# Performance work log

Hardware: AMD Instinct MI355X
Metric: run time of the kernel (lower is better)

The kernel has to match this reference:

```python
import jax, jax.numpy as jnp
import numpy as np

DIM = 768
HEADS = 12
B, NV, NQ, NA = 32, 100, 32, 32


def setup_inputs() -> dict:
    key = jax.random.key(0)
    ks = jax.random.split(key, 18)
    inp = {
        "v": jax.random.normal(ks[0], (B, NV, DIM), jnp.float32),
        "q": jax.random.normal(ks[1], (B, NQ, DIM), jnp.float32),
        "a": jax.random.normal(ks[2], (B, NA, DIM), jnp.float32),
        "v_mask": jax.random.randint(ks[3], (B, NV), 0, 2, jnp.int32),
        "q_mask": jax.random.randint(ks[4], (B, NQ), 0, 2, jnp.int32),
        "a_mask": jax.random.randint(ks[5], (B, NA), 0, 2, jnp.int32),
    }
    names = ["Wv", "bv", "Wq", "bq", "Wa", "ba", "Wvo", "bvo", "Wqo", "bqo", "Wao", "bao"]
    for i, n in enumerate(names):
        shape = (DIM, DIM) if n.startswith("W") else (DIM,)
        inp[n] = jax.random.normal(ks[6 + i], shape, jnp.float32) * 0.02
    return inp


def _heads(x):
    # (B, S, DIM) -> (B, H, S, W)
    b, s, _ = x.shape
    return x.reshape(b, s, HEADS, DIM // HEADS).transpose(0, 2, 1, 3)


def reference(v, q, a, v_mask, q_mask, a_mask,
              Wv, bv, Wq, bq, Wa, ba, Wvo, bvo, Wqo, bqo, Wao, bao):
    # projections; note: *_out projections are applied to the already-projected tensors
    vp = v @ Wv + bv
    qp = q @ Wq + bq
    ap = a @ Wa + ba
    vo = vp @ Wvo + bvo
    qo = qp @ Wqo + bqo
    ao = ap @ Wao + bao

    vh, qh, ah = _heads(vp), _heads(qp), _heads(ap)          # (B,H,S,W)
    voh, qoh, aoh = _heads(vo), _heads(qo), _heads(ao)

    dh = DIM // HEADS
    scale = 1.0 / float(np.sqrt(dh))
    # trilinear scores: (B,H,V,Q,A)
    att = jnp.einsum('bhvw,bhqw,bhaw->bhvqa', vh, qh, ah) * scale
    att = att - 10000.0 * v_mask[:, None, :, None, None].astype(att.dtype)
    att = att - 10000.0 * q_mask[:, None, None, :, None].astype(att.dtype)
    att = att - 10000.0 * a_mask[:, None, None, None, :].astype(att.dtype)

    # softmax over the flattened joint (V*Q*A) axis, per (batch, head)
    att = jax.nn.softmax(att.reshape(B, HEADS, NV * NQ * NA), axis=-1)
    att = att.reshape(B, HEADS, NV, NQ, NA)  # dropout: eval mode (identity)

    v_out = jnp.einsum('bhvqa,bhvw->bvhw', att, voh).reshape(B, NV, DIM)
    q_out = jnp.einsum('bhvqa,bhqw->bqhw', att, qoh).reshape(B, NQ, DIM)
    a_out = jnp.einsum('bhvqa,bhaw->bahw', att, aoh).reshape(B, NA, DIM)
    return (v_out, q_out, a_out)
```

## Files before the change

kernel.cpp:

```cpp
#include <hip/hip_runtime.h>
#include <hip/hip_bf16.h>

#define DIM 768
#define NH  12
#define HW  64
#define BB  32
#define NV  100
#define NQ  32
#define NA  32

#define VP_ELEMS (BB * NV * DIM)
#define QP_ELEMS (BB * NQ * DIM)
#define AP_ELEMS (BB * NA * DIM)
#define S1 (VP_ELEMS)
#define S2 (S1 + QP_ELEMS)
#define STOT (S2 + AP_ELEMS)
#define WELEMS (DIM * DIM)
#define NBH (BB * NH)
#define PREP_BLOCKS (864 + BB)
#define NROWS (BB * (NV + NQ + NA))

typedef __attribute__((ext_vector_type(8))) short     bf16x8;
typedef __attribute__((ext_vector_type(8))) unsigned short u16x8;
typedef __attribute__((ext_vector_type(4))) float     f32x4;

__device__ __forceinline__ float bf16r(float x) {
    return __bfloat162float(__float2bfloat16(x));
}
__device__ __forceinline__ unsigned short f2bu(float x) {
    __hip_bfloat16 h = __float2bfloat16(x);
    return *reinterpret_cast<unsigned short*>(&h);
}
__device__ __forceinline__ float bu2f(unsigned short u) {
    union { unsigned int i; float f; } c;
    c.i = ((unsigned int)u) << 16;
    return c.f;
}

__global__ __launch_bounds__(256) void prep(
    const float* __restrict__ W0, const float* __restrict__ W1,
    const float* __restrict__ W2, const float* __restrict__ W3,
    const float* __restrict__ W4, const float* __restrict__ W5,
    unsigned short* __restrict__ WtAll,
    const int* __restrict__ vmask, const int* __restrict__ qmask, const int* __restrict__ amask,
    int* __restrict__ vidx_g, int* __restrict__ qidx_g, int* __restrict__ aidx_g,
    int* __restrict__ vbase_g, int* __restrict__ qbase_g, int* __restrict__ abase_g,
    int* __restrict__ rv_list, int* __restrict__ rq_list, int* __restrict__ ra_list,
    int* __restrict__ tot_g,
    float* __restrict__ out)
{
    const int tid = threadIdx.x;

#pragma unroll
    for (int it = 0; it < 5; ++it) {
        const int e4 = blockIdx.x * 256 + tid + it * (PREP_BLOCKS * 256);
        const int i = e4 * 4;
        if (i < STOT) *(float4*)&out[i] = float4{0.f, 0.f, 0.f, 0.f};
    }

    if (blockIdx.x < 864) {
        __shared__ float tile[64][65];
        const int widx = blockIdx.x / 144;
        const int t    = blockIdx.x % 144;
        const int tr = t / 12, tc = t % 12;
        const float* W = (widx == 0) ? W0 : (widx == 1) ? W1 : (widx == 2) ? W2
                       : (widx == 3) ? W3 : (widx == 4) ? W4 : W5;
        unsigned short* Wt = WtAll + (size_t)widx * WELEMS;
        const int c = tid & 63, r4 = tid >> 6;
#pragma unroll
        for (int it = 0; it < 16; ++it) {
            int r = it * 4 + r4;
            tile[r][c] = W[(size_t)(tr * 64 + r) * DIM + tc * 64 + c];
        }
        __syncthreads();
#pragma unroll
        for (int it = 0; it < 16; ++it) {
            int r = it * 4 + r4;
            Wt[(size_t)(tc * 64 + r) * DIM + tr * 64 + c] = f2bu(tile[c][r]);
        }
        return;
    }

    const int b = blockIdx.x - 864;
    __shared__ int cv[BB], cq[BB], ca[BB];
    __shared__ int bs[3];

    if (tid < BB) {
        int s = 0;
        for (int i = 0; i < NV; ++i) s += (vmask[tid * NV + i] == 0);
        cv[tid] = s;
    } else if (tid >= 64 && tid < 64 + BB) {
        const int bb = tid - 64;
        int s = 0;
        for (int i = 0; i < NQ; ++i) s += (qmask[bb * NQ + i] == 0);
        cq[bb] = s;
    } else if (tid >= 128 && tid < 128 + BB) {
        const int bb = tid - 128;
        int s = 0;
        for (int i = 0; i < NA; ++i) s += (amask[bb * NA + i] == 0);
        ca[bb] = s;
    }
    __syncthreads();

    if (tid == 0) {
        int sv = 0, sq = 0, sa = 0;
        for (int j = 0; j < b; ++j) { sv += cv[j]; sq += cq[j]; sa += ca[j]; }
        bs[0] = sv; bs[1] = sq; bs[2] = sa;
        vbase_g[b] = sv; qbase_g[b] = sq; abase_g[b] = sa;
    }
    if (b == 0 && tid == 1) {
        int sv = 0, sq = 0, sa = 0;
        for (int j = 0; j < BB; ++j) { sv += cv[j]; sq += cq[j]; sa += ca[j]; }
        vbase_g[BB] = sv; qbase_g[BB] = sq; abase_g[BB] = sa;
        tot_g[0] = sv; tot_g[1] = sq; tot_g[2] = sa;
    }
    __syncthreads();
    const int basev = bs[0], baseq = bs[1], basea = bs[2];

    const int lane = tid & 63, w = tid >> 6;
    __shared__ int c0sh;
    const bool mv = (tid < NV) && (vmask[b * NV + tid] == 0);
    const unsigned long long bal = __ballot(mv);
    const int pre = __popcll(bal & ((1ull << lane) - 1ull));
    if (w == 0 && lane == 0) c0sh = __popcll(bal);
    __syncthreads();
    const int vbloc = (w == 0) ? 0 : c0sh;
    if (mv) {
        vidx_g[b * NV + vbloc + pre] = tid;
        rv_list[basev + vbloc + pre] = b * NV + tid;
    }
    const bool mq = (w == 0) && (lane < NQ) && (qmask[b * NQ + lane] == 0);
    const unsigned long long balq = __ballot(mq);
    if (mq) {
        const int preq = __popcll(balq & ((1ull << lane) - 1ull));
        qidx_g[b * NQ + preq] = lane;
        rq_list[baseq + preq] = b * NQ + lane;
    }
    const bool ma = (w == 1) && (lane < NA) && (amask[b * NA + lane] == 0);
    const unsigned long long bala = __ballot(ma);
    if (ma) {
        const int prea = __popcll(bala & ((1ull << lane) - 1ull));
        aidx_g[b * NA + prea] = lane;
        ra_list[basea + prea] = b * NA + lane;
    }
}

__global__ __launch_bounds__(256) void gemm_proj(
    const float* __restrict__ X0, const float* __restrict__ X1, const float* __restrict__ X2,
    const unsigned short* __restrict__ W0, const unsigned short* __restrict__ W1,
    const unsigned short* __restrict__ W2,
    const float* __restrict__ c0, const float* __restrict__ c1, const float* __restrict__ c2,
    unsigned short* __restrict__ Y0, unsigned short* __restrict__ Y1,
    unsigned short* __restrict__ Y2,
    const int* __restrict__ rv_list, const int* __restrict__ rq_list, const int* __restrict__ ra_list,
    const int* __restrict__ tot_g)
{
    __shared__ unsigned short As[64 * 32];
    __shared__ unsigned short Bs[128 * 32];

    const int t = blockIdx.x;
    int set, loc;
    if (t < 300)      { set = 0; loc = t; }
    else if (t < 396) { set = 1; loc = t - 300; }
    else              { set = 2; loc = t - 396; }
    const int tm = loc / 6, tn = loc % 6;
    const int cnt = tot_g[set];
    const int bm = tm * 64, bn = tn * 128;
    if (bm >= cnt) return;

    const float* Xf          = (set == 0) ? X0 : (set == 1) ? X1 : X2;
    const unsigned short* Wt = (set == 0) ? W0 : (set == 1) ? W1 : W2;
    const float* bias        = (set == 0) ? c0 : (set == 1) ? c1 : c2;
    unsigned short* Y        = (set == 0) ? Y0 : (set == 1) ? Y1 : Y2;
    const int* rlist         = (set == 0) ? rv_list : (set == 1) ? rq_list : ra_list;

    const int tid = threadIdx.x, lane = tid & 63, wave = tid >> 6;
    const int col = lane & 15, rg = lane >> 4;

    const int arow = tid >> 2, akc = (tid & 3) << 3;
    const int brow = tid >> 1, bkc = (tid & 1) << 4;
    const int grow = bm + arow;
    const int asrc = (grow < cnt) ? rlist[grow] : 0;

    f32x4 acc[4][2] = {};

    for (int k0 = 0; k0 < DIM; k0 += 32) {
        u16x8 u = {};
        if (grow < cnt) {
            const float4 f0 = *(const float4*)&Xf[(size_t)asrc * DIM + k0 + akc];
            const float4 f1 = *(const float4*)&Xf[(size_t)asrc * DIM + k0 + akc + 4];
            u[0] = f2bu(f0.x); u[1] = f2bu(f0.y); u[2] = f2bu(f0.z); u[3] = f2bu(f0.w);
            u[4] = f2bu(f1.x); u[5] = f2bu(f1.y); u[6] = f2bu(f1.z); u[7] = f2bu(f1.w);
        }
        *(u16x8*)&As[arow * 32 + akc] = u;
        *(u16x8*)&Bs[brow * 32 + bkc] =
            *(const u16x8*)&Wt[(size_t)(bn + brow) * DIM + k0 + bkc];
        *(u16x8*)&Bs[brow * 32 + bkc + 8] =
            *(const u16x8*)&Wt[(size_t)(bn + brow) * DIM + k0 + bkc + 8];
        __syncthreads();

        bf16x8 af[4], bfr[2];
#pragma unroll
        for (int mi = 0; mi < 4; ++mi)
            af[mi] = *(const bf16x8*)&As[(mi * 16 + col) * 32 + rg * 8];
#pragma unroll
        for (int ni = 0; ni < 2; ++ni)
            bfr[ni] = *(const bf16x8*)&Bs[(wave * 32 + ni * 16 + col) * 32 + rg * 8];
#pragma unroll
        for (int mi = 0; mi < 4; ++mi)
#pragma unroll
            for (int ni = 0; ni < 2; ++ni)
                acc[mi][ni] = __builtin_amdgcn_mfma_f32_16x16x32_bf16(
                    af[mi], bfr[ni], acc[mi][ni], 0, 0, 0);
        __syncthreads();
    }

#pragma unroll
    for (int mi = 0; mi < 4; ++mi) {
#pragma unroll
        for (int r = 0; r < 4; ++r) {
            const int m = bm + mi * 16 + rg * 4 + r;
            if (m >= cnt) continue;
#pragma unroll
            for (int ni = 0; ni < 2; ++ni) {
                const int n = bn + wave * 32 + ni * 16 + col;
                Y[(size_t)m * DIM + n] = f2bu(acc[mi][ni][r] + bias[n]);
            }
        }
    }
}

__global__ __launch_bounds__(256, 2) void outmm_marginal(
    const unsigned short* __restrict__ vpb, const unsigned short* __restrict__ qpb,
    const unsigned short* __restrict__ apb,
    const unsigned short* __restrict__ W3, const unsigned short* __restrict__ W4,
    const unsigned short* __restrict__ W5,
    const float* __restrict__ bvo, const float* __restrict__ bqo, const float* __restrict__ bao,
    unsigned short* __restrict__ ov, unsigned short* __restrict__ oq, unsigned short* __restrict__ oa,
    const int* __restrict__ vbase_g, const int* __restrict__ qbase_g, const int* __restrict__ abase_g,
    const int* __restrict__ vidx_g, const int* __restrict__ qidx_g, const int* __restrict__ aidx_g,
    float* __restrict__ pv, float* __restrict__ pq, float* __restrict__ pa,
    const int* __restrict__ tot_g)
{
    const int tid = threadIdx.x, lane = tid & 63, wave = tid >> 6;
    const int col = lane & 15, rg = lane >> 4;

    if (blockIdx.x < 492) {
        __shared__ unsigned short As[64 * 32];
        __shared__ unsigned short Bs[128 * 32];
        const int t = blockIdx.x;
        int set, loc;
        if (t < 300)      { set = 0; loc = t; }
        else if (t < 396) { set = 1; loc = t - 300; }
        else              { set = 2; loc = t - 396; }
        const int tm = loc / 6, tn = loc % 6;
        const int cnt = tot_g[set];
        const int bm = tm * 64, bn = tn * 128;
        if (bm >= cnt) return;

        const unsigned short* Xb = (set == 0) ? vpb : (set == 1) ? qpb : apb;
        const unsigned short* Wt = (set == 0) ? W3 : (set == 1) ? W4 : W5;
        const float* bias        = (set == 0) ? bvo : (set == 1) ? bqo : bao;
        unsigned short* Y        = (set == 0) ? ov : (set == 1) ? oq : oa;

        const int arow = tid >> 2, akc = (tid & 3) << 3;
        const int brow = tid >> 1, bkc = (tid & 1) << 4;
        const int grow = bm + arow;

        f32x4 acc[4][2] = {};
        for (int k0 = 0; k0 < DIM; k0 += 32) {
            *(u16x8*)&As[arow * 32 + akc] =
                *(const u16x8*)&Xb[(size_t)grow * DIM + k0 + akc];
            *(u16x8*)&Bs[brow * 32 + bkc] =
                *(const u16x8*)&Wt[(size_t)(bn + brow) * DIM + k0 + bkc];
            *(u16x8*)&Bs[brow * 32 + bkc + 8] =
                *(const u16x8*)&Wt[(size_t)(bn + brow) * DIM + k0 + bkc + 8];
            __syncthreads();

            bf16x8 af[4], bfr[2];
#pragma unroll
            for (int mi = 0; mi < 4; ++mi)
                af[mi] = *(const bf16x8*)&As[(mi * 16 + col) * 32 + rg * 8];
#pragma unroll
            for (int ni = 0; ni < 2; ++ni)
                bfr[ni] = *(const bf16x8*)&Bs[(wave * 32 + ni * 16 + col) * 32 + rg * 8];
#pragma unroll
            for (int mi = 0; mi < 4; ++mi)
#pragma unroll
                for (int ni = 0; ni < 2; ++ni)
                    acc[mi][ni] = __builtin_amdgcn_mfma_f32_16x16x32_bf16(
                        af[mi], bfr[ni], acc[mi][ni], 0, 0, 0);
            __syncthreads();
        }

#pragma unroll
        for (int mi = 0; mi < 4; ++mi) {
#pragma unroll
            for (int r = 0; r < 4; ++r) {
                const int m = bm + mi * 16 + rg * 4 + r;
                if (m >= cnt) continue;
#pragma unroll
                for (int ni = 0; ni < 2; ++ni) {
                    const int n = bn + wave * 32 + ni * 16 + col;
                    Y[(size_t)m * DIM + n] = f2bu(acc[mi][ni][r] + bias[n]);
                }
            }
        }
        return;
    }

    const int bh = blockIdx.x - 492;
    const int b = bh / NH, h = bh % NH;

    __shared__ unsigned short vhs[112 * 72];
    __shared__ unsigned short qhs[NQ * 72];
    __shared__ unsigned short ahs[NA * 72];
    __shared__ float aoff[NA];
    __shared__ float pv_sh[112], pa_sh[NA], pq_sh[NQ];
    __shared__ float zsh;

    const int vb0 = vbase_g[b], vcnt = vbase_g[b + 1] - vb0;
    const int qb0 = qbase_g[b], qcnt = qbase_g[b + 1] - qb0;
    const int ab0 = abase_g[b], acnt = abase_g[b + 1] - ab0;

    if (tid < 112) pv_sh[tid] = 0.f;
    if (tid < NA)  { aoff[tid] = (tid < acnt) ? 0.f : -200.f; pa_sh[tid] = 0.f; }

    for (int i = tid >> 3; i < vcnt; i += 32) {
        const int c = tid & 7;
        *(u16x8*)&vhs[i * 72 + c * 8] =
            *(const u16x8*)&vpb[(size_t)(vb0 + i) * DIM + h * 64 + c * 8];
    }
    {
        const int pr = vcnt + (tid >> 3);
        if ((tid >> 3) < 16 && pr < 112) {
            const int c = tid & 7;
            u16x8 z = {};
            *(u16x8*)&vhs[pr * 72 + c * 8] = z;
        }
    }
    for (int i = tid >> 3; i < qcnt; i += 32) {
        const int c = tid & 7;
        *(u16x8*)&qhs[i * 72 + c * 8] =
            *(const u16x8*)&qpb[(size_t)(qb0 + i) * DIM + h * 64 + c * 8];
    }
    for (int i = tid >> 3; i < acnt; i += 32) {
        const int c = tid & 7;
        *(u16x8*)&ahs[i * 72 + c * 8] =
            *(const u16x8*)&apb[(size_t)(ab0 + i) * DIM + h * 64 + c * 8];
    }
    {
        const int pr = acnt + (tid >> 3);
        if ((tid >> 3) < 16 && pr < NA) {
            const int c = tid & 7;
            u16x8 z = {};
            *(u16x8*)&ahs[pr * 72 + c * 8] = z;
        }
    }
    __syncthreads();

    const int nvt = (vcnt + 15) >> 4;
    const int nat = (acnt + 15) >> 4;

    float pvacc[7][4] = {};
    float za0 = 0.f, za1 = 0.f;
    const float sc2 = 0.125f * 1.44269504088896f;

    for (int qs = wave; qs < qcnt; qs += 4) {
        float zq = 0.f;
#pragma unroll
        for (int ah = 0; ah < 2; ++ah) {
            if (ah < nat) {
                const int ai = (ah << 4) + col;
                const u16x8 qv0 = *(const u16x8*)&qhs[qs * 72 + rg * 8];
                const u16x8 qv1 = *(const u16x8*)&qhs[qs * 72 + 32 + rg * 8];
                const u16x8 av0 = *(const u16x8*)&ahs[ai * 72 + rg * 8];
                const u16x8 av1 = *(const u16x8*)&ahs[ai * 72 + 32 + rg * 8];
                bf16x8 bf0, bf1;
#pragma unroll
                for (int j = 0; j < 8; ++j) {
                    bf0[j] = (short)f2bu(bu2f(qv0[j]) * bu2f(av0[j]));
                    bf1[j] = (short)f2bu(bu2f(qv1[j]) * bu2f(av1[j]));
                }
                const float poff = aoff[ai];
                float ts = 0.f;
#pragma unroll
                for (int vt = 0; vt < 7; ++vt) {
                    if (vt < nvt) {
                        const bf16x8 a0 = *(const bf16x8*)&vhs[(vt * 16 + col) * 72 + rg * 8];
                        const bf16x8 a1 = *(const bf16x8*)&vhs[(vt * 16 + col) * 72 + 32 + rg * 8];
                        f32x4 acc = {};
                        acc = __builtin_amdgcn_mfma_f32_16x16x32_bf16(a0, bf0, acc, 0, 0, 0);
                        acc = __builtin_amdgcn_mfma_f32_16x16x32_bf16(a1, bf1, acc, 0, 0, 0);
                        if ((vt + 1) * 16 <= vcnt) {
#pragma unroll
                            for (int r = 0; r < 4; ++r) {
                                const float e = exp2f(fmaf(acc[r], sc2, poff));
                                pvacc[vt][r] += e;
                                ts += e;
                            }
                        } else {
#pragma unroll
                            for (int r = 0; r < 4; ++r) {
                                const float off = (vt * 16 + rg * 4 + r < vcnt) ? poff : -200.f;
                                const float e = exp2f(fmaf(acc[r], sc2, off));
                                pvacc[vt][r] += e;
                                ts += e;
                            }
                        }
                    }
                }
                if (ah) za1 += ts; else za0 += ts;
                zq += ts;
            }
        }
        zq += __shfl_xor(zq, 1);  zq += __shfl_xor(zq, 2);  zq += __shfl_xor(zq, 4);
        zq += __shfl_xor(zq, 8);  zq += __shfl_xor(zq, 16); zq += __shfl_xor(zq, 32);
        if (lane == 0) pq_sh[qs] = zq;
    }

#pragma unroll
    for (int vt = 0; vt < 7; ++vt) {
        if (vt < nvt) {
#pragma unroll
            for (int r = 0; r < 4; ++r) {
                float x = pvacc[vt][r];
                x += __shfl_xor(x, 1); x += __shfl_xor(x, 2);
                x += __shfl_xor(x, 4); x += __shfl_xor(x, 8);
                if (col == 0) atomicAdd(&pv_sh[vt * 16 + rg * 4 + r], x);
            }
        }
    }
    {
        float x = za0;
        x += __shfl_xor(x, 16); x += __shfl_xor(x, 32);
        if (rg == 0) atomicAdd(&pa_sh[col], x);
        float y = za1;
        y += __shfl_xor(y, 16); y += __shfl_xor(y, 32);
        if (rg == 0) atomicAdd(&pa_sh[16 + col], y);
    }
    __syncthreads();

    if (tid < 64) {
        float x = (lane < qcnt) ? pq_sh[lane] : 0.f;
        x += __shfl_xor(x, 1); x += __shfl_xor(x, 2); x += __shfl_xor(x, 4);
        x += __shfl_xor(x, 8); x += __shfl_xor(x, 16); x += __shfl_xor(x, 32);
        if (lane == 0) zsh = x;
    }
    if (tid < NV) pv[bh * NV + tid] = 0.f;
    if (tid < NQ) pq[bh * NQ + tid] = 0.f;
    if (tid < NA) pa[bh * NA + tid] = 0.f;
    __syncthreads();
    const float invZ = 1.0f / zsh;
    if (tid < vcnt) pv[bh * NV + vidx_g[b * NV + tid]] = pv_sh[tid] * invZ;
    if (tid < qcnt) pq[bh * NQ + qidx_g[b * NQ + tid]] = pq_sh[tid] * invZ;
    if (tid < acnt) pa[bh * NA + aidx_g[b * NA + tid]] = pa_sh[tid] * invZ;
}

__global__ __launch_bounds__(192) void scale_out(
    const unsigned short* __restrict__ ov, const unsigned short* __restrict__ oq,
    const unsigned short* __restrict__ oa,
    const float* __restrict__ pv, const float* __restrict__ pq, const float* __restrict__ pa,
    const int* __restrict__ rv_list, const int* __restrict__ rq_list, const int* __restrict__ ra_list,
    const int* __restrict__ tot_g, float* __restrict__ out)
{
    const int t0 = tot_g[0], t1 = tot_g[1], t2 = tot_g[2];
    int m = blockIdx.x;
    const unsigned short* ob; const float* mg; const int* rl; int S; float* os;
    if (m < t0)           { ob = ov; mg = pv; rl = rv_list; S = NV; os = out; }
    else if (m < t0 + t1) { m -= t0; ob = oq; mg = pq; rl = rq_list; S = NQ; os = out + S1; }
    else if (m < t0 + t1 + t2) { m -= t0 + t1; ob = oa; mg = pa; rl = ra_list; S = NA; os = out + S2; }
    else return;

    const int src = rl[m];
    const int bb = src / S, ss = src - bb * S;
    const int n = threadIdx.x * 4;
    const int h = n >> 6;
    const float mgv = mg[(bb * NH + h) * S + ss];
    const ushort4 u = *(const ushort4*)&ob[(size_t)m * DIM + n];
    float4 o;
    o.x = bf16r(bu2f(u.x) * mgv);
    o.y = bf16r(bu2f(u.y) * mgv);
    o.z = bf16r(bu2f(u.z) * mgv);
    o.w = bf16r(bu2f(u.w) * mgv);
    *(float4*)&os[(size_t)src * DIM + n] = o;
}

extern "C" void kernel_launch(void* const* d_in, const int* in_sizes, int n_in,
                              void* d_out, int out_size, void* d_ws, size_t ws_size,
                              hipStream_t stream)
{
    const float* v     = (const float*)d_in[0];
    const float* q     = (const float*)d_in[1];
    const float* a     = (const float*)d_in[2];
    const int*   vmask = (const int*)d_in[3];
    const int*   qmask = (const int*)d_in[4];
    const int*   amask = (const int*)d_in[5];
    const float* Wv  = (const float*)d_in[6];
    const float* bv  = (const float*)d_in[7];
    const float* Wq  = (const float*)d_in[8];
    const float* bq  = (const float*)d_in[9];
    const float* Wa  = (const float*)d_in[10];
    const float* ba  = (const float*)d_in[11];
    const float* Wvo = (const float*)d_in[12];
    const float* bvo = (const float*)d_in[13];
    const float* Wqo = (const float*)d_in[14];
    const float* bqo = (const float*)d_in[15];
    const float* Wao = (const float*)d_in[16];
    const float* bao = (const float*)d_in[17];
    float* out = (float*)d_out;

    unsigned short* wsu = (unsigned short*)d_ws;
    unsigned short* WtAll = wsu;
    unsigned short* vpb   = WtAll + 6 * WELEMS;
    unsigned short* qpb   = vpb + VP_ELEMS;
    unsigned short* apb   = qpb + QP_ELEMS;
    unsigned short* ov    = apb + AP_ELEMS;
    unsigned short* oq    = ov + VP_ELEMS;
    unsigned short* oa    = oq + QP_ELEMS;
    float* fbase   = (float*)(oa + AP_ELEMS);
    float* pv      = fbase;
    float* pq      = pv + NBH * NV;
    float* pa      = pq + NBH * NQ;
    int* vidx_g    = (int*)(pa + NBH * NA);
    int* qidx_g    = vidx_g + BB * NV;
    int* aidx_g    = qidx_g + BB * NQ;
    int* vbase_g   = aidx_g + BB * NA;
    int* qbase_g   = vbase_g + BB + 1;
    int* abase_g   = qbase_g + BB + 1;
    int* rv_list   = abase_g + BB + 1;
    int* rq_list   = rv_list + BB * NV;
    int* ra_list   = rq_list + BB * NQ;
    int* tot_g     = ra_list + BB * NA;

    prep<<<dim3(PREP_BLOCKS), dim3(256), 0, stream>>>(
        Wv, Wq, Wa, Wvo, Wqo, Wao, WtAll,
        vmask, qmask, amask,
        vidx_g, qidx_g, aidx_g, vbase_g, qbase_g, abase_g,
        rv_list, rq_list, ra_list, tot_g, out);

    gemm_proj<<<dim3(492), dim3(256), 0, stream>>>(
        v, q, a,
        WtAll + 0 * WELEMS, WtAll + 1 * WELEMS, WtAll + 2 * WELEMS,
        bv, bq, ba,
        vpb, qpb, apb,
        rv_list, rq_list, ra_list, tot_g);

    outmm_marginal<<<dim3(492 + NBH), dim3(256), 0, stream>>>(
        vpb, qpb, apb,
        WtAll + 3 * WELEMS, WtAll + 4 * WELEMS, WtAll + 5 * WELEMS,
        bvo, bqo, bao,
        ov, oq, oa,
        vbase_g, qbase_g, abase_g,
        vidx_g, qidx_g, aidx_g,
        pv, pq, pa, tot_g);

    scale_out<<<dim3(NROWS), dim3(192), 0, stream>>>(
        ov, oq, oa, pv, pq, pa,
        rv_list, rq_list, ra_list, tot_g, out);
}
```

Measured before the change: 67.86 us.

## Defer output-weight conversion and output zeroing into the projection GEMM launch

The prep kernel now converts only the three input projection weights. The conversion of the three output weights and the zeroing of the output buffer move into extra blocks of the gemm_proj launch, so they run alongside the projection GEMM. This shortens the serial prep stage on the critical path. In exchange, the GEMM blocks share the GPU with the conversion blocks and also take on part of the zeroing stores.

Measured after the change: 65.87 us. 2.9% less time.

```diff
diff --git a/kernel.cpp b/kernel.cpp
--- a/kernel.cpp
+++ b/kernel.cpp
@@ -17,8 +17,8 @@
 #define STOT (S2 + AP_ELEMS)
 #define WELEMS (DIM * DIM)
 #define NBH (BB * NH)
-#define PREP_BLOCKS (864 + BB)
 #define NROWS (BB * (NV + NQ + NA))
+#define P2_BLOCKS (492 + 432)
 
 typedef __attribute__((ext_vector_type(8))) short     bf16x8;
 typedef __attribute__((ext_vector_type(8))) unsigned short u16x8;
@@ -37,51 +37,45 @@
     return c.f;
 }
 
+__device__ __forceinline__ void conv_tile(
+    const float* __restrict__ W, unsigned short* __restrict__ Wt, int t, int tid)
+{
+    __shared__ float tile[64][65];
+    const int tr = t / 12, tc = t % 12;
+    const int c = tid & 63, r4 = tid >> 6;
+#pragma unroll
+    for (int it = 0; it < 16; ++it) {
+        int r = it * 4 + r4;
+        tile[r][c] = W[(size_t)(tr * 64 + r) * DIM + tc * 64 + c];
+    }
+    __syncthreads();
+#pragma unroll
+    for (int it = 0; it < 16; ++it) {
+        int r = it * 4 + r4;
+        Wt[(size_t)(tc * 64 + r) * DIM + tr * 64 + c] = f2bu(tile[c][r]);
+    }
+}
+
 __global__ __launch_bounds__(256) void prep(
     const float* __restrict__ W0, const float* __restrict__ W1,
-    const float* __restrict__ W2, const float* __restrict__ W3,
-    const float* __restrict__ W4, const float* __restrict__ W5,
+    const float* __restrict__ W2,
     unsigned short* __restrict__ WtAll,
     const int* __restrict__ vmask, const int* __restrict__ qmask, const int* __restrict__ amask,
     int* __restrict__ vidx_g, int* __restrict__ qidx_g, int* __restrict__ aidx_g,
     int* __restrict__ vbase_g, int* __restrict__ qbase_g, int* __restrict__ abase_g,
     int* __restrict__ rv_list, int* __restrict__ rq_list, int* __restrict__ ra_list,
-    int* __restrict__ tot_g,
-    float* __restrict__ out)
+    int* __restrict__ tot_g)
 {
     const int tid = threadIdx.x;
 
-#pragma unroll
-    for (int it = 0; it < 5; ++it) {
-        const int e4 = blockIdx.x * 256 + tid + it * (PREP_BLOCKS * 256);
-        const int i = e4 * 4;
-        if (i < STOT) *(float4*)&out[i] = float4{0.f, 0.f, 0.f, 0.f};
-    }
-
-    if (blockIdx.x < 864) {
-        __shared__ float tile[64][65];
+    if (blockIdx.x < 432) {
         const int widx = blockIdx.x / 144;
-        const int t    = blockIdx.x % 144;
-        const int tr = t / 12, tc = t % 12;
-        const float* W = (widx == 0) ? W0 : (widx == 1) ? W1 : (widx == 2) ? W2
-                       : (widx == 3) ? W3 : (widx == 4) ? W4 : W5;
-        unsigned short* Wt = WtAll + (size_t)widx * WELEMS;
-        const int c = tid & 63, r4 = tid >> 6;
-#pragma unroll
-        for (int it = 0; it < 16; ++it) {
-            int r = it * 4 + r4;
-            tile[r][c] = W[(size_t)(tr * 64 + r) * DIM + tc * 64 + c];
-        }
-        __syncthreads();
-#pragma unroll
-        for (int it = 0; it < 16; ++it) {
-            int r = it * 4 + r4;
-            Wt[(size_t)(tc * 64 + r) * DIM + tr * 64 + c] = f2bu(tile[c][r]);
-        }
+        const float* W = (widx == 0) ? W0 : (widx == 1) ? W1 : W2;
+        conv_tile(W, WtAll + (size_t)widx * WELEMS, blockIdx.x % 144, tid);
         return;
     }
 
-    const int b = blockIdx.x - 864;
+    const int b = blockIdx.x - 432;
     __shared__ int cv[BB], cq[BB], ca[BB];
     __shared__ int bs[3];
 
@@ -147,14 +141,32 @@
 
 __global__ __launch_bounds__(256) void gemm_proj(
     const float* __restrict__ X0, const float* __restrict__ X1, const float* __restrict__ X2,
-    const unsigned short* __restrict__ W0, const unsigned short* __restrict__ W1,
-    const unsigned short* __restrict__ W2,
+    const float* __restrict__ W3, const float* __restrict__ W4, const float* __restrict__ W5,
+    unsigned short* __restrict__ WtAll,
     const float* __restrict__ c0, const float* __restrict__ c1, const float* __restrict__ c2,
     unsigned short* __restrict__ Y0, unsigned short* __restrict__ Y1,
     unsigned short* __restrict__ Y2,
     const int* __restrict__ rv_list, const int* __restrict__ rq_list, const int* __restrict__ ra_list,
-    const int* __restrict__ tot_g)
+    const int* __restrict__ tot_g,
+    float* __restrict__ out)
 {
+    const int tid = threadIdx.x;
+
+#pragma unroll
+    for (int it = 0; it < 5; ++it) {
+        const int e4 = blockIdx.x * 256 + tid + it * (P2_BLOCKS * 256);
+        const int i = e4 * 4;
+        if (i < STOT) *(float4*)&out[i] = float4{0.f, 0.f, 0.f, 0.f};
+    }
+
+    if (blockIdx.x >= 492) {
+        const int cblk = blockIdx.x - 492;
+        const int widx = 3 + cblk / 144;
+        const float* W = (widx == 3) ? W3 : (widx == 4) ? W4 : W5;
+        conv_tile(W, WtAll + (size_t)widx * WELEMS, cblk % 144, tid);
+        return;
+    }
+
     __shared__ unsigned short As[64 * 32];
     __shared__ unsigned short Bs[128 * 32];
 
@@ -169,12 +181,12 @@
     if (bm >= cnt) return;
 
     const float* Xf          = (set == 0) ? X0 : (set == 1) ? X1 : X2;
-    const unsigned short* Wt = (set == 0) ? W0 : (set == 1) ? W1 : W2;
+    const unsigned short* Wt = WtAll + (size_t)set * WELEMS;
     const float* bias        = (set == 0) ? c0 : (set == 1) ? c1 : c2;
     unsigned short* Y        = (set == 0) ? Y0 : (set == 1) ? Y1 : Y2;
     const int* rlist         = (set == 0) ? rv_list : (set == 1) ? rq_list : ra_list;
 
-    const int tid = threadIdx.x, lane = tid & 63, wave = tid >> 6;
+    const int lane = tid & 63, wave = tid >> 6;
     const int col = lane & 15, rg = lane >> 4;
 
     const int arow = tid >> 2, akc = (tid & 3) << 3;
@@ -533,18 +545,18 @@
     int* ra_list   = rq_list + BB * NQ;
     int* tot_g     = ra_list + BB * NA;
 
-    prep<<<dim3(PREP_BLOCKS), dim3(256), 0, stream>>>(
-        Wv, Wq, Wa, Wvo, Wqo, Wao, WtAll,
+    prep<<<dim3(432 + BB), dim3(256), 0, stream>>>(
+        Wv, Wq, Wa, WtAll,
         vmask, qmask, amask,
         vidx_g, qidx_g, aidx_g, vbase_g, qbase_g, abase_g,
-        rv_list, rq_list, ra_list, tot_g, out);
-
-    gemm_proj<<<dim3(492), dim3(256), 0, stream>>>(
+        rv_list, rq_list, ra_list, tot_g);
+
+    gemm_proj<<<dim3(P2_BLOCKS), dim3(256), 0, stream>>>(
         v, q, a,
-        WtAll + 0 * WELEMS, WtAll + 1 * WELEMS, WtAll + 2 * WELEMS,
+        Wvo, Wqo, Wao, WtAll,
         bv, bq, ba,
         vpb, qpb, apb,
-        rv_list, rq_list, ra_list, tot_g);
+        rv_list, rq_list, ra_list, tot_g, out);
 
     outmm_marginal<<<dim3(492 + NBH), dim3(256), 0, stream>>>(
         vpb, qpb, apb,
```
